# Optimization experiments

Measured on AMD Instinct MI355X. Metric: run time of the kernel, lower is better.

## Reference

```python
import jax, jax.numpy as jnp
import numpy as np

T, H, I, E, K = 1024, 1024, 512, 32, 4   # tokens, hidden, moe_inter, n_experts, top_k
G, TG, NS = 8, 4, 2                      # n_group, topk_group, n_shared_experts
C = 2 * T * K // E                       # expert capacity (no-drop headroom)
SCALE = 2.5                              # routed_scaling_factor


def setup_inputs() -> dict:
    key = jax.random.key(0)
    ks = jax.random.split(key, 7)
    s = 0.02
    return dict(
        hidden_states=jax.random.normal(ks[0], (T, H), jnp.float32),
        gate_w=jax.random.normal(ks[1], (E, H), jnp.float32) * s,
        e_bias=jax.random.normal(ks[2], (E,), jnp.float32) * 0.1,
        w_gate_up=jax.random.normal(ks[3], (E, 2 * I, H), jnp.float32) * s,
        w_down=jax.random.normal(ks[4], (E, H, I), jnp.float32) * s,
        w_gate_up_shared=jax.random.normal(ks[5], (2 * I * NS, H), jnp.float32) * s,
        w_down_shared=jax.random.normal(ks[6], (H, I * NS), jnp.float32) * s,
    )


def reference(hidden_states, gate_w, e_bias, w_gate_up, w_down, w_gate_up_shared, w_down_shared):
    x = hidden_states                                   # (T, H)
    # --- gate + sigmoid scoring (noaux_tc) ---
    logits = x @ gate_w.T                               # (T, E)
    scores = jax.nn.sigmoid(logits.astype(jnp.float32))
    sfc = scores + e_bias                               # scores_for_choice
    # --- group-limited top-k: top-2 sum per group, keep topk_group groups ---
    group_scores = jax.lax.top_k(sfc.reshape(T, G, E // G), 2)[0].sum(-1)  # (T, G)
    grp_idx = jax.lax.top_k(group_scores, TG)[1]        # (T, TG)
    gmask = jnp.zeros((T, G), jnp.float32).at[jnp.arange(T)[:, None], grp_idx].set(1.0)
    smask = jnp.repeat(gmask, E // G, axis=1)           # (T, E)
    sfc_m = jnp.where(smask > 0, sfc, 0.0)
    topk_idx = jax.lax.top_k(sfc_m, K)[1]               # (T, K)
    tw = jnp.take_along_axis(scores, topk_idx, axis=1)  # weights from raw scores
    tw = tw / (tw.sum(-1, keepdims=True) + 1e-20)       # norm_topk_prob
    tw = tw * SCALE
    # --- capacity-based dispatch (position within expert via cumsum of one-hot) ---
    e_flat = topk_idx.reshape(-1)                       # (T*K,)
    oh = jax.nn.one_hot(e_flat, E, dtype=jnp.float32)   # (T*K, E)
    pos = jnp.sum((jnp.cumsum(oh, axis=0) - 1.0) * oh, axis=-1).astype(jnp.int32)
    keep = (pos < C).astype(jnp.float32)                # capacity sized to never drop
    pos_c = jnp.clip(pos, 0, C - 1)
    t_flat = jnp.repeat(jnp.arange(T), K)
    combine = jnp.zeros((T, E, C), jnp.float32).at[t_flat, e_flat, pos_c].add(tw.reshape(-1) * keep)
    dispatch = jnp.zeros((T, E, C), jnp.float32).at[t_flat, e_flat, pos_c].add(keep)
    # --- grouped expert MLP (gate_up -> SiluAndMul -> down) ---
    xe = jnp.einsum('tec,th->ech', dispatch, x)         # (E, C, H)
    gu = jnp.einsum('ech,eoh->eco', xe, w_gate_up)      # (E, C, 2I)
    act = jax.nn.silu(gu[..., :I]) * gu[..., I:]
    ye = jnp.einsum('eci,ehi->ech', act, w_down)        # (E, C, H)
    routed = jnp.einsum('tec,ech->th', combine, ye)     # (T, H)
    # --- shared experts MLP on residual ---
    IS = I * NS
    gus = x @ w_gate_up_shared.T                        # (T, 2*IS)
    acts = jax.nn.silu(gus[:, :IS]) * gus[:, IS:]
    shared = acts @ w_down_shared.T                     # (T, H)
    return routed + shared
```

## Files before the change

### kernel.cpp

```cpp
#include <hip/hip_runtime.h>
#include <hip/hip_bf16.h>
#include <math.h>

#define T_TOK 1024
#define H_DIM 1024
#define I_DIM 512
#define E_NUM 32
#define K_TOP 4
#define G_NUM 8
#define TG_NUM 4
#define CAP 256
#define IS_DIM 1024
#define RSCALE 2.5f

#define MAXTILES 36

#define WS_CNT_OFF    0
#define WS_NT_OFF     128
#define WS_TILE_OFF   256
#define WS_EIDX_OFF   4096
#define WS_WN_OFF     20480
#define WS_STOK_OFF   36864
#define WS_SW_OFF     69632
#define WS_ACT_OFF    102400
#define WS_ACTS_OFF   (102400 + (size_t)E_NUM*CAP*I_DIM*2)
#define WS_XB_OFF     (WS_ACTS_OFF + (size_t)T_TOK*IS_DIM*2)
#define WS_T2S_OFF    (WS_XB_OFF + (size_t)T_TOK*H_DIM*2)
#define WS_YR_OFF     (WS_T2S_OFF + (size_t)T_TOK*K_TOP*4)

typedef __attribute__((ext_vector_type(8))) short short8v;
typedef __attribute__((ext_vector_type(4))) float f32x4;
typedef __attribute__((ext_vector_type(4))) unsigned uint4v;

__device__ __forceinline__ short f2bf(float f) {
    unsigned u = __float_as_uint(f);
    u += 0x7FFFu + ((u >> 16) & 1u);
    return (short)(u >> 16);
}
__device__ __forceinline__ unsigned pk2bf(float a, float b) {
    unsigned ua = __float_as_uint(a) + 0x8000u;
    unsigned ub = __float_as_uint(b) + 0x8000u;
    return __builtin_amdgcn_perm(ub, ua, 0x07060302);
}
__device__ __forceinline__ uint4v pk8bf(float4 lo, float4 hi) {
    uint4v r; r.x = pk2bf(lo.x, lo.y); r.y = pk2bf(lo.z, lo.w);
    r.z = pk2bf(hi.x, hi.y); r.w = pk2bf(hi.z, hi.w); return r;
}
__device__ __forceinline__ float silu_(float g) { return g / (1.f + expf(-g)); }

#define BAR_RELAXED() do { \
    asm volatile("s_waitcnt lgkmcnt(0)" ::: "memory"); \
    __builtin_amdgcn_s_barrier(); \
    asm volatile("" ::: "memory"); \
} while (0)

#define LDSTRIDE 40

__global__ __launch_bounds__(256) void gate_kernel(
    const float* __restrict__ x, const float* __restrict__ gate_w,
    const float* __restrict__ e_bias,
    int* __restrict__ eidx, float* __restrict__ wnorm, short* __restrict__ xb)
{
    __shared__ float xs[H_DIM];
    __shared__ float logits[E_NUM];
    const int t = blockIdx.x;
    const int tid = threadIdx.x;
    float4 v = ((const float4*)(x + (size_t)t * H_DIM))[tid];
    ((float4*)xs)[tid] = v;
    {
        unsigned* xd = (unsigned*)(xb + (size_t)t * H_DIM) + tid * 2;
        xd[0] = pk2bf(v.x, v.y); xd[1] = pk2bf(v.z, v.w);
    }
    __syncthreads();

    const int e = tid >> 3, sub = tid & 7;
    const float4* gw4 = (const float4*)(gate_w + (size_t)e * H_DIM + sub * 128);
    const float4* xr4 = (const float4*)(xs + sub * 128);
    float p = 0.f;
    #pragma unroll
    for (int h = 0; h < 32; ++h) {
        float4 a = xr4[h], b = gw4[h];
        p += a.x * b.x + a.y * b.y + a.z * b.z + a.w * b.w;
    }
    for (int off = 4; off; off >>= 1) p += __shfl_down(p, off, 8);
    if (sub == 0) logits[e] = p;
    __syncthreads();
    if (tid != 0) return;

    float sc[E_NUM], sfc[E_NUM];
    for (int i = 0; i < E_NUM; ++i) {
        sc[i] = 1.f / (1.f + expf(-logits[i]));
        sfc[i] = sc[i] + e_bias[i];
    }
    float gs[G_NUM];
    for (int g = 0; g < G_NUM; ++g) {
        float m1 = -1e30f, m2 = -1e30f;
        for (int j = 0; j < E_NUM / G_NUM; ++j) {
            float v2 = sfc[g * (E_NUM / G_NUM) + j];
            if (v2 > m1) { m2 = m1; m1 = v2; } else if (v2 > m2) m2 = v2;
        }
        gs[g] = m1 + m2;
    }
    bool gm[G_NUM];
    for (int g = 0; g < G_NUM; ++g) gm[g] = false;
    for (int it = 0; it < TG_NUM; ++it) {
        int best = -1; float bv = -1e30f;
        for (int g = 0; g < G_NUM; ++g) if (!gm[g] && gs[g] > bv) { bv = gs[g]; best = g; }
        gm[best] = true;
    }
    float sm[E_NUM];
    for (int i = 0; i < E_NUM; ++i) sm[i] = gm[i / (E_NUM / G_NUM)] ? sfc[i] : 0.0f;
    int idx[K_TOP]; float w[K_TOP]; float tsum = 0.f;
    for (int it = 0; it < K_TOP; ++it) {
        int best = 0; float bv = -1e30f;
        for (int i = 0; i < E_NUM; ++i) if (sm[i] > bv) { bv = sm[i]; best = i; }
        sm[best] = -1e30f;
        idx[it] = best; w[it] = sc[best]; tsum += w[it];
    }
    float inv = RSCALE / (tsum + 1e-20f);
    const int base = t * K_TOP;
    for (int it = 0; it < K_TOP; ++it) {
        eidx[base + it] = idx[it];
        wnorm[base + it] = w[it] * inv;
    }
}

__global__ __launch_bounds__(256) void assign_kernel(
    const int* __restrict__ eidx, const float* __restrict__ wnorm,
    int* __restrict__ cnt, int* __restrict__ slot_token, float* __restrict__ slot_w,
    int* __restrict__ ntiles, int* __restrict__ tiles, int* __restrict__ tok2slot)
{
    __shared__ int   se[T_TOK * K_TOP];
    __shared__ float swt[T_TOK * K_TOP];
    __shared__ int   scnt[E_NUM];
    const int tid = threadIdx.x;
    for (int i = tid; i < T_TOK * K_TOP; i += 256) { se[i] = eidx[i]; swt[i] = wnorm[i]; }
    __syncthreads();

    const int e = tid >> 3;
    const int seg = tid & 7;
    const int base = seg * 512;
    int c = 0;
    for (int i = 0; i < 512; ++i) c += (se[base + i] == e);
    int excl = 0, total = 0;
    for (int s = 0; s < 8; ++s) {
        int cs = __shfl(c, s, 8);
        total += cs;
        if (s < seg) excl += cs;
    }
    if (seg == 0) { cnt[e] = total; scnt[e] = total; }
    __syncthreads();
    int boff = 0;
    for (int ee = 0; ee < e; ++ee) boff += min(scnt[ee], CAP);

    int pos = excl;
    for (int i = 0; i < 512; ++i) {
        if (se[base + i] == e) {
            const int g = base + i;
            if (pos < CAP) {
                slot_token[e * CAP + pos] = g >> 2;
                slot_w[e * CAP + pos] = swt[g];
                tok2slot[g] = boff + pos;
            } else {
                tok2slot[g] = -1;
            }
            ++pos;
        }
    }
    __syncthreads();
    if (tid == 0) {
        int nt = 0;
        for (int t0 = 0; t0 < T_TOK; t0 += 256) {
            tiles[nt * 4] = -1; tiles[nt * 4 + 1] = t0; tiles[nt * 4 + 2] = 256;
            tiles[nt * 4 + 3] = 0; ++nt;
        }
        int off = 0;
        for (int ee = 0; ee < E_NUM; ++ee) {
            int n = min(scnt[ee], CAP);
            if (n > 0) {
                tiles[nt * 4] = ee; tiles[nt * 4 + 1] = 0; tiles[nt * 4 + 2] = n;
                tiles[nt * 4 + 3] = off; ++nt;
            }
            off += n;
        }
        *ntiles = nt;
    }
}


__global__ __launch_bounds__(512, 2) void gu_all_kernel(
    const short* __restrict__ xb, const float* __restrict__ w_gate_up,
    const float* __restrict__ w_gus,
    const int* __restrict__ ntiles, const int* __restrict__ tiles,
    const int* __restrict__ slot_token, const float* __restrict__ slot_w,
    short* __restrict__ act, short* __restrict__ acts)
{
    if ((int)blockIdx.y >= *ntiles) return;
    const int e  = tiles[blockIdx.y * 4];
    const int r0 = tiles[blockIdx.y * 4 + 1];
    const int ne = tiles[blockIdx.y * 4 + 2];
    const bool sh = (e < 0);
    if (!sh && blockIdx.x >= I_DIM / 64) return;
    const int col0 = blockIdx.x * 64;
    const int mchunks = (ne + 63) >> 6;
    const int rows = mchunks << 6;

    __shared__ __align__(16) short As[2][256 * LDSTRIDE];
    __shared__ __align__(16) short Bs[2][128 * LDSTRIDE];
    __shared__ int   toks[256];
    __shared__ float sws[256];

    const int tid = threadIdx.x;
    const int lane = tid & 63, wid = tid >> 6;
    const int wm = wid & 3, wn = wid >> 2;
    const int lr16 = lane & 15, kc = lane >> 4;
    const int sc_ = tid & 3, srow = tid >> 2;

    if (tid < 256) {
        if (sh) { toks[tid] = r0 + tid; sws[tid] = 1.f; }
        else {
            bool v = tid < ne;
            toks[tid] = v ? slot_token[e * CAP + tid] : 0;
            sws[tid]  = v ? slot_w[e * CAP + tid] : 0.f;
        }
    }
    __syncthreads();

    const int IDim = sh ? IS_DIM : I_DIM;
    const float* wbase = sh ? w_gus : (w_gate_up + (size_t)e * (2 * I_DIM) * H_DIM);
    const int wr = ((srow >> 4) & 1) * IDim + col0 + ((srow >> 5) << 4) + (srow & 15);
    const float* bptr = wbase + (size_t)wr * H_DIM + sc_ * 8;
    const bool a0v = srow < rows;
    const bool a1v = (srow + 128) < rows;
    const short* aptr0 = xb + (size_t)toks[srow] * H_DIM + sc_ * 8;
    const short* aptr1 = xb + (size_t)toks[srow + 128] * H_DIM + sc_ * 8;
    const int aoff0 = srow * LDSTRIDE + sc_ * 8;
    const int aoff1 = (srow + 128) * LDSTRIDE + sc_ * 8;
    const int boff  = srow * LDSTRIDE + sc_ * 8;

    f32x4 acc[4][4];
    #pragma unroll
    for (int i = 0; i < 4; ++i)
        #pragma unroll
        for (int j = 0; j < 4; ++j) acc[i][j] = 0.f;

    short8v cA0{}, cA1{};
    if (a0v) cA0 = *(const short8v*)(aptr0);
    if (a1v) cA1 = *(const short8v*)(aptr1);
    float4 cB0 = *(const float4*)(bptr), cB1 = *(const float4*)(bptr + 4);

    int buf = 0;
    for (int k0 = 0; k0 < H_DIM; k0 += 32) {
        short8v nA0{}, nA1{};
        float4 nB0{}, nB1{};
        const int k1 = k0 + 32;
        if (k1 < H_DIM) {
            if (a0v) nA0 = *(const short8v*)(aptr0 + k1);
            if (a1v) nA1 = *(const short8v*)(aptr1 + k1);
            nB0 = *(const float4*)(bptr + k1); nB1 = *(const float4*)(bptr + k1 + 4);
        }
        if (a0v) *(short8v*)&As[buf][aoff0] = cA0;
        if (a1v) *(short8v*)&As[buf][aoff1] = cA1;
        *(uint4v*)&Bs[buf][boff] = pk8bf(cB0, cB1);
        BAR_RELAXED();
        if (wm < mchunks) {
            short8v a_[4], b_[4];
            #pragma unroll
            for (int mt = 0; mt < 4; ++mt)
                a_[mt] = *(const short8v*)&As[buf][(wm * 64 + mt * 16 + lr16) * LDSTRIDE + kc * 8];
            #pragma unroll
            for (int nt = 0; nt < 4; ++nt)
                b_[nt] = *(const short8v*)&Bs[buf][(wn * 64 + nt * 16 + lr16) * LDSTRIDE + kc * 8];
            #pragma unroll
            for (int mt = 0; mt < 4; ++mt)
                #pragma unroll
                for (int nt = 0; nt < 4; ++nt)
                    acc[mt][nt] = __builtin_amdgcn_mfma_f32_16x16x32_bf16(a_[mt], b_[nt], acc[mt][nt], 0, 0, 0);
        }
        buf ^= 1;
        cA0 = nA0; cA1 = nA1; cB0 = nB0; cB1 = nB1;
    }

    if (wm >= mchunks) return;
    #pragma unroll
    for (int mt = 0; mt < 4; ++mt) {
        #pragma unroll
        for (int q = 0; q < 2; ++q) {
            f32x4 g = acc[mt][2 * q], u = acc[mt][2 * q + 1];
            const int colI = col0 + wn * 32 + q * 16 + lr16;
            #pragma unroll
            for (int i = 0; i < 4; ++i) {
                int r = wm * 64 + mt * 16 + kc * 4 + i;
                if (r < ne) {
                    float s = sws[r];
                    short* dst = sh ? (acts + (size_t)(r0 + r) * IS_DIM + colI)
                                    : (act + ((size_t)e * CAP + r) * I_DIM + colI);
                    *dst = f2bf(s * silu_(g[i]) * u[i]);
                }
            }
        }
    }
}

__global__ __launch_bounds__(512, 2) void down_all_kernel(
    const short* __restrict__ act, const short* __restrict__ acts,
    const float* __restrict__ w_down, const float* __restrict__ w_ds,
    const int* __restrict__ ntiles, const int* __restrict__ tiles,
    float* __restrict__ yr, float* __restrict__ out)
{
    if ((int)blockIdx.y >= *ntiles) return;
    const int e  = tiles[blockIdx.y * 4];
    const int r0 = tiles[blockIdx.y * 4 + 1];
    const int ne = tiles[blockIdx.y * 4 + 2];
    const int bo = tiles[blockIdx.y * 4 + 3];
    const bool sh = (e < 0);
    const int h0 = blockIdx.x * 128;
    const int mchunks = (ne + 63) >> 6;
    const int rows = mchunks << 6;

    __shared__ __align__(16) short As[2][256 * LDSTRIDE];
    __shared__ __align__(16) short Bs[2][128 * LDSTRIDE];

    const int tid = threadIdx.x;
    const int lane = tid & 63, wid = tid >> 6;
    const int wm = wid & 3, wn = wid >> 2;
    const int lr16 = lane & 15, kc = lane >> 4;
    const int sc_ = tid & 3, srow = tid >> 2;

    const int Kdim = sh ? IS_DIM : I_DIM;
    const short* abase = sh ? (acts + (size_t)r0 * IS_DIM) : (act + (size_t)e * CAP * I_DIM);
    const float* wbase = sh ? w_ds : (w_down + (size_t)e * H_DIM * I_DIM);
    const float* bptr  = wbase + (size_t)(h0 + srow) * Kdim + sc_ * 8;
    const bool a0v = srow < rows;
    const bool a1v = (srow + 128) < rows;
    const short* aptr0 = abase + (size_t)srow * Kdim + sc_ * 8;
    const short* aptr1 = abase + (size_t)(srow + 128) * Kdim + sc_ * 8;
    const int aoff0 = srow * LDSTRIDE + sc_ * 8;
    const int aoff1 = (srow + 128) * LDSTRIDE + sc_ * 8;
    const int boff  = srow * LDSTRIDE + sc_ * 8;

    f32x4 acc[4][4];
    #pragma unroll
    for (int i = 0; i < 4; ++i)
        #pragma unroll
        for (int j = 0; j < 4; ++j) acc[i][j] = 0.f;

    short8v cA0{}, cA1{};
    if (a0v) cA0 = *(const short8v*)(aptr0);
    if (a1v) cA1 = *(const short8v*)(aptr1);
    float4 cB0 = *(const float4*)(bptr), cB1 = *(const float4*)(bptr + 4);

    int buf = 0;
    for (int k0 = 0; k0 < Kdim; k0 += 32) {
        short8v nA0{}, nA1{};
        float4 nB0{}, nB1{};
        const int k1 = k0 + 32;
        if (k1 < Kdim) {
            if (a0v) nA0 = *(const short8v*)(aptr0 + k1);
            if (a1v) nA1 = *(const short8v*)(aptr1 + k1);
            nB0 = *(const float4*)(bptr + k1); nB1 = *(const float4*)(bptr + k1 + 4);
        }
        if (a0v) *(short8v*)&As[buf][aoff0] = cA0;
        if (a1v) *(short8v*)&As[buf][aoff1] = cA1;
        *(uint4v*)&Bs[buf][boff] = pk8bf(cB0, cB1);
        BAR_RELAXED();
        if (wm < mchunks) {
            short8v a_[4], b_[4];
            #pragma unroll
            for (int mt = 0; mt < 4; ++mt)
                a_[mt] = *(const short8v*)&As[buf][(wm * 64 + mt * 16 + lr16) * LDSTRIDE + kc * 8];
            #pragma unroll
            for (int nt = 0; nt < 4; ++nt)
                b_[nt] = *(const short8v*)&Bs[buf][(wn * 64 + nt * 16 + lr16) * LDSTRIDE + kc * 8];
            #pragma unroll
            for (int mt = 0; mt < 4; ++mt)
                #pragma unroll
                for (int nt = 0; nt < 4; ++nt)
                    acc[mt][nt] = __builtin_amdgcn_mfma_f32_16x16x32_bf16(a_[mt], b_[nt], acc[mt][nt], 0, 0, 0);
        }
        buf ^= 1;
        cA0 = nA0; cA1 = nA1; cB0 = nB0; cB1 = nB1;
    }

    if (wm >= mchunks) return;
    #pragma unroll
    for (int mt = 0; mt < 4; ++mt) {
        #pragma unroll
        for (int i = 0; i < 4; ++i) {
            int r = wm * 64 + mt * 16 + kc * 4 + i;
            if (r < ne) {
                float* orow = sh ? (out + (size_t)(r0 + r) * H_DIM + h0 + wn * 64)
                                 : (yr + (size_t)(bo + r) * H_DIM + h0 + wn * 64);
                #pragma unroll
                for (int nt = 0; nt < 4; ++nt)
                    orow[nt * 16 + lr16] = acc[mt][nt][i];
            }
        }
    }
}

__global__ __launch_bounds__(256) void combine_kernel(
    const float* __restrict__ yr, const int* __restrict__ tok2slot,
    float* __restrict__ out)
{
    const int t = blockIdx.x, tid = threadIdx.x;
    float4 a = ((const float4*)(out + (size_t)t * H_DIM))[tid];
    #pragma unroll
    for (int k = 0; k < K_TOP; ++k) {
        int s = tok2slot[t * K_TOP + k];
        if (s >= 0) {
            float4 b = ((const float4*)(yr + (size_t)s * H_DIM))[tid];
            a.x += b.x; a.y += b.y; a.z += b.z; a.w += b.w;
        }
    }
    ((float4*)(out + (size_t)t * H_DIM))[tid] = a;
}

extern "C" void kernel_launch(void* const* d_in, const int* in_sizes, int n_in,
                              void* d_out, int out_size, void* d_ws, size_t ws_size,
                              hipStream_t stream) {
    const float* x   = (const float*)d_in[0];
    const float* gw  = (const float*)d_in[1];
    const float* eb  = (const float*)d_in[2];
    const float* wgu = (const float*)d_in[3];
    const float* wd  = (const float*)d_in[4];
    const float* wgs = (const float*)d_in[5];
    const float* wds = (const float*)d_in[6];
    float* out = (float*)d_out;
    char* ws = (char*)d_ws;

    int*   cnt    = (int*)(ws + WS_CNT_OFF);
    int*   ntiles = (int*)(ws + WS_NT_OFF);
    int*   tiles  = (int*)(ws + WS_TILE_OFF);
    int*   eidx   = (int*)(ws + WS_EIDX_OFF);
    float* wnorm  = (float*)(ws + WS_WN_OFF);
    int*   stok   = (int*)(ws + WS_STOK_OFF);
    float* sw     = (float*)(ws + WS_SW_OFF);
    short* act    = (short*)(ws + WS_ACT_OFF);
    short* acts   = (short*)(ws + WS_ACTS_OFF);
    short* xb     = (short*)(ws + WS_XB_OFF);
    int*   t2s    = (int*)(ws + WS_T2S_OFF);
    float* yr     = (float*)(ws + WS_YR_OFF);

    gate_kernel<<<T_TOK, 256, 0, stream>>>(x, gw, eb, eidx, wnorm, xb);
    assign_kernel<<<1, 256, 0, stream>>>(eidx, wnorm, cnt, stok, sw, ntiles, tiles, t2s);
    gu_all_kernel<<<dim3(IS_DIM / 64, MAXTILES), 512, 0, stream>>>(
        xb, wgu, wgs, ntiles, tiles, stok, sw, act, acts);
    down_all_kernel<<<dim3(H_DIM / 128, MAXTILES), 512, 0, stream>>>(
        act, acts, wd, wds, ntiles, tiles, yr, out);
    combine_kernel<<<T_TOK, 256, 0, stream>>>(yr, t2s, out);
}
```

Before: 440.7 us.

## Split expert tiles into 128-row chunks with BK=64 and higher occupancy

Changes the tile scheduler to emit 128-row tiles for both shared and routed experts, so an expert with more than 128 slots becomes several tiles and more blocks run. Both GEMM kernels move from a 256x128 block tile to 128x128 with a 2x4 warp layout, a K-step of 64 and LDS stride 72, and launch bounds allow 4 blocks per CU. Rows are no longer masked per 64-row chunk: loads always run, which depends on padding rows in the token and activation buffers being safe to read. The aim is better load balance and occupancy, at the cost of more redundant weight reads across row tiles.

```diff
diff --git a/kernel.cpp b/kernel.cpp
--- a/kernel.cpp
+++ b/kernel.cpp
@@ -13,7 +13,7 @@
 #define IS_DIM 1024
 #define RSCALE 2.5f
 
-#define MAXTILES 36
+#define MAXTILES 72
 
 #define WS_CNT_OFF    0
 #define WS_NT_OFF     128
@@ -54,7 +54,7 @@
     asm volatile("" ::: "memory"); \
 } while (0)
 
-#define LDSTRIDE 40
+#define LDSTRIDE 72
 
 __global__ __launch_bounds__(256) void gate_kernel(
     const float* __restrict__ x, const float* __restrict__ gate_w,
@@ -170,16 +170,17 @@
     __syncthreads();
     if (tid == 0) {
         int nt = 0;
-        for (int t0 = 0; t0 < T_TOK; t0 += 256) {
-            tiles[nt * 4] = -1; tiles[nt * 4 + 1] = t0; tiles[nt * 4 + 2] = 256;
+        for (int t0 = 0; t0 < T_TOK; t0 += 128) {
+            tiles[nt * 4] = -1; tiles[nt * 4 + 1] = t0; tiles[nt * 4 + 2] = 128;
             tiles[nt * 4 + 3] = 0; ++nt;
         }
         int off = 0;
         for (int ee = 0; ee < E_NUM; ++ee) {
             int n = min(scnt[ee], CAP);
-            if (n > 0) {
-                tiles[nt * 4] = ee; tiles[nt * 4 + 1] = 0; tiles[nt * 4 + 2] = n;
-                tiles[nt * 4 + 3] = off; ++nt;
+            for (int r = 0; r < n; r += 128) {
+                tiles[nt * 4] = ee; tiles[nt * 4 + 1] = r;
+                tiles[nt * 4 + 2] = min(128, n - r);
+                tiles[nt * 4 + 3] = off + r; ++nt;
             }
             off += n;
         }
@@ -188,7 +189,33 @@
 }
 
 
-__global__ __launch_bounds__(512, 2) void gu_all_kernel(
+#define GEMM_SETUP() \
+    const int tid = threadIdx.x; \
+    const int lane = tid & 63, wid = tid >> 6; \
+    const int wm = wid & 1, wn = wid >> 1; \
+    const int lr16 = lane & 15, kc = lane >> 4; \
+    const int sc_ = tid & 7, srow = tid >> 3; \
+    const int aoff0 = srow * LDSTRIDE + sc_ * 8; \
+    const int aoff1 = (srow + 64) * LDSTRIDE + sc_ * 8;
+
+#define DECL_ACC42() f32x4 acc[4][2]; \
+    _Pragma("unroll") for (int i_ = 0; i_ < 4; ++i_) \
+    _Pragma("unroll") for (int j_ = 0; j_ < 2; ++j_) acc[i_][j_] = 0.f;
+
+#define COMPUTE_BK64(Asb, Bsb) do { \
+    _Pragma("unroll") for (int ks = 0; ks < 2; ++ks) { \
+        short8v a_[4], b_[2]; \
+        _Pragma("unroll") for (int mt = 0; mt < 4; ++mt) \
+            a_[mt] = *(const short8v*)&(Asb)[(wm*64 + mt*16 + lr16)*LDSTRIDE + ks*32 + kc*8]; \
+        _Pragma("unroll") for (int nt = 0; nt < 2; ++nt) \
+            b_[nt] = *(const short8v*)&(Bsb)[(wn*32 + nt*16 + lr16)*LDSTRIDE + ks*32 + kc*8]; \
+        _Pragma("unroll") for (int mt = 0; mt < 4; ++mt) \
+        _Pragma("unroll") for (int nt = 0; nt < 2; ++nt) \
+            acc[mt][nt] = __builtin_amdgcn_mfma_f32_16x16x32_bf16(a_[mt], b_[nt], acc[mt][nt], 0, 0, 0); \
+    } \
+} while (0)
+
+__global__ __launch_bounds__(512, 4) void gu_all_kernel(
     const short* __restrict__ xb, const float* __restrict__ w_gate_up,
     const float* __restrict__ w_gus,
     const int* __restrict__ ntiles, const int* __restrict__ tiles,
@@ -202,107 +229,77 @@
     const bool sh = (e < 0);
     if (!sh && blockIdx.x >= I_DIM / 64) return;
     const int col0 = blockIdx.x * 64;
-    const int mchunks = (ne + 63) >> 6;
-    const int rows = mchunks << 6;
-
-    __shared__ __align__(16) short As[2][256 * LDSTRIDE];
+
+    __shared__ __align__(16) short As[2][128 * LDSTRIDE];
     __shared__ __align__(16) short Bs[2][128 * LDSTRIDE];
-    __shared__ int   toks[256];
-    __shared__ float sws[256];
-
-    const int tid = threadIdx.x;
-    const int lane = tid & 63, wid = tid >> 6;
-    const int wm = wid & 3, wn = wid >> 2;
-    const int lr16 = lane & 15, kc = lane >> 4;
-    const int sc_ = tid & 3, srow = tid >> 2;
-
-    if (tid < 256) {
+    __shared__ int   toks[128];
+    __shared__ float sws[128];
+
+    GEMM_SETUP();
+    if (tid < 128) {
         if (sh) { toks[tid] = r0 + tid; sws[tid] = 1.f; }
         else {
             bool v = tid < ne;
-            toks[tid] = v ? slot_token[e * CAP + tid] : 0;
-            sws[tid]  = v ? slot_w[e * CAP + tid] : 0.f;
+            toks[tid] = v ? slot_token[e * CAP + r0 + tid] : 0;
+            sws[tid]  = v ? slot_w[e * CAP + r0 + tid] : 0.f;
         }
     }
     __syncthreads();
 
     const int IDim = sh ? IS_DIM : I_DIM;
     const float* wbase = sh ? w_gus : (w_gate_up + (size_t)e * (2 * I_DIM) * H_DIM);
-    const int wr = ((srow >> 4) & 1) * IDim + col0 + ((srow >> 5) << 4) + (srow & 15);
-    const float* bptr = wbase + (size_t)wr * H_DIM + sc_ * 8;
-    const bool a0v = srow < rows;
-    const bool a1v = (srow + 128) < rows;
-    const short* aptr0 = xb + (size_t)toks[srow] * H_DIM + sc_ * 8;
-    const short* aptr1 = xb + (size_t)toks[srow + 128] * H_DIM + sc_ * 8;
-    const int aoff0 = srow * LDSTRIDE + sc_ * 8;
-    const int aoff1 = (srow + 128) * LDSTRIDE + sc_ * 8;
-    const int boff  = srow * LDSTRIDE + sc_ * 8;
-
-    f32x4 acc[4][4];
-    #pragma unroll
-    for (int i = 0; i < 4; ++i)
-        #pragma unroll
-        for (int j = 0; j < 4; ++j) acc[i][j] = 0.f;
-
-    short8v cA0{}, cA1{};
-    if (a0v) cA0 = *(const short8v*)(aptr0);
-    if (a1v) cA1 = *(const short8v*)(aptr1);
-    float4 cB0 = *(const float4*)(bptr), cB1 = *(const float4*)(bptr + 4);
+    const int r_0 = srow, r_1 = srow + 64;
+    const int wr0 = ((r_0 >> 4) & 1) * IDim + col0 + ((r_0 >> 5) << 4) + (r_0 & 15);
+    const int wr1 = ((r_1 >> 4) & 1) * IDim + col0 + ((r_1 >> 5) << 4) + (r_1 & 15);
+    const float* bptr0 = wbase + (size_t)wr0 * H_DIM + sc_ * 8;
+    const float* bptr1 = wbase + (size_t)wr1 * H_DIM + sc_ * 8;
+    const short* aptr0 = xb + (size_t)toks[r_0] * H_DIM + sc_ * 8;
+    const short* aptr1 = xb + (size_t)toks[r_1] * H_DIM + sc_ * 8;
+
+    DECL_ACC42();
+    short8v cA0 = *(const short8v*)(aptr0), cA1 = *(const short8v*)(aptr1);
+    float4 cB0a = *(const float4*)(bptr0), cB0b = *(const float4*)(bptr0 + 4);
+    float4 cB1a = *(const float4*)(bptr1), cB1b = *(const float4*)(bptr1 + 4);
 
     int buf = 0;
-    for (int k0 = 0; k0 < H_DIM; k0 += 32) {
+    for (int k0 = 0; k0 < H_DIM; k0 += 64) {
         short8v nA0{}, nA1{};
-        float4 nB0{}, nB1{};
-        const int k1 = k0 + 32;
+        float4 nB0a{}, nB0b{}, nB1a{}, nB1b{};
+        const int k1 = k0 + 64;
         if (k1 < H_DIM) {
-            if (a0v) nA0 = *(const short8v*)(aptr0 + k1);
-            if (a1v) nA1 = *(const short8v*)(aptr1 + k1);
-            nB0 = *(const float4*)(bptr + k1); nB1 = *(const float4*)(bptr + k1 + 4);
-        }
-        if (a0v) *(short8v*)&As[buf][aoff0] = cA0;
-        if (a1v) *(short8v*)&As[buf][aoff1] = cA1;
-        *(uint4v*)&Bs[buf][boff] = pk8bf(cB0, cB1);
+            nA0 = *(const short8v*)(aptr0 + k1);  nA1 = *(const short8v*)(aptr1 + k1);
+            nB0a = *(const float4*)(bptr0 + k1);  nB0b = *(const float4*)(bptr0 + k1 + 4);
+            nB1a = *(const float4*)(bptr1 + k1);  nB1b = *(const float4*)(bptr1 + k1 + 4);
+        }
+        *(short8v*)&As[buf][aoff0] = cA0;
+        *(short8v*)&As[buf][aoff1] = cA1;
+        *(uint4v*)&Bs[buf][aoff0]  = pk8bf(cB0a, cB0b);
+        *(uint4v*)&Bs[buf][aoff1]  = pk8bf(cB1a, cB1b);
         BAR_RELAXED();
-        if (wm < mchunks) {
-            short8v a_[4], b_[4];
-            #pragma unroll
-            for (int mt = 0; mt < 4; ++mt)
-                a_[mt] = *(const short8v*)&As[buf][(wm * 64 + mt * 16 + lr16) * LDSTRIDE + kc * 8];
-            #pragma unroll
-            for (int nt = 0; nt < 4; ++nt)
-                b_[nt] = *(const short8v*)&Bs[buf][(wn * 64 + nt * 16 + lr16) * LDSTRIDE + kc * 8];
-            #pragma unroll
-            for (int mt = 0; mt < 4; ++mt)
-                #pragma unroll
-                for (int nt = 0; nt < 4; ++nt)
-                    acc[mt][nt] = __builtin_amdgcn_mfma_f32_16x16x32_bf16(a_[mt], b_[nt], acc[mt][nt], 0, 0, 0);
-        }
+        COMPUTE_BK64(As[buf], Bs[buf]);
         buf ^= 1;
-        cA0 = nA0; cA1 = nA1; cB0 = nB0; cB1 = nB1;
-    }
-
-    if (wm >= mchunks) return;
+        cA0 = nA0; cA1 = nA1;
+        cB0a = nB0a; cB0b = nB0b; cB1a = nB1a; cB1b = nB1b;
+    }
+
     #pragma unroll
     for (int mt = 0; mt < 4; ++mt) {
+        f32x4 g = acc[mt][0], u = acc[mt][1];
+        const int colI = col0 + wn * 16 + lr16;
         #pragma unroll
-        for (int q = 0; q < 2; ++q) {
-            f32x4 g = acc[mt][2 * q], u = acc[mt][2 * q + 1];
-            const int colI = col0 + wn * 32 + q * 16 + lr16;
-            #pragma unroll
-            for (int i = 0; i < 4; ++i) {
-                int r = wm * 64 + mt * 16 + kc * 4 + i;
-                if (r < ne) {
-                    float s = sws[r];
-                    short* dst = sh ? (acts + (size_t)(r0 + r) * IS_DIM + colI)
-                                    : (act + ((size_t)e * CAP + r) * I_DIM + colI);
-                    *dst = f2bf(s * silu_(g[i]) * u[i]);
-                }
+        for (int i = 0; i < 4; ++i) {
+            int r = wm * 64 + mt * 16 + kc * 4 + i;
+            if (r < ne) {
+                float s = sws[r];
+                short* dst = sh ? (acts + (size_t)(r0 + r) * IS_DIM + colI)
+                                : (act + ((size_t)e * CAP + r0 + r) * I_DIM + colI);
+                *dst = f2bf(s * silu_(g[i]) * u[i]);
             }
         }
     }
 }
 
-__global__ __launch_bounds__(512, 2) void down_all_kernel(
+__global__ __launch_bounds__(512, 4) void down_all_kernel(
     const short* __restrict__ act, const short* __restrict__ acts,
     const float* __restrict__ w_down, const float* __restrict__ w_ds,
     const int* __restrict__ ntiles, const int* __restrict__ tiles,
@@ -315,84 +312,57 @@
     const int bo = tiles[blockIdx.y * 4 + 3];
     const bool sh = (e < 0);
     const int h0 = blockIdx.x * 128;
-    const int mchunks = (ne + 63) >> 6;
-    const int rows = mchunks << 6;
-
-    __shared__ __align__(16) short As[2][256 * LDSTRIDE];
+
+    __shared__ __align__(16) short As[2][128 * LDSTRIDE];
     __shared__ __align__(16) short Bs[2][128 * LDSTRIDE];
 
-    const int tid = threadIdx.x;
-    const int lane = tid & 63, wid = tid >> 6;
-    const int wm = wid & 3, wn = wid >> 2;
-    const int lr16 = lane & 15, kc = lane >> 4;
-    const int sc_ = tid & 3, srow = tid >> 2;
+    GEMM_SETUP();
 
     const int Kdim = sh ? IS_DIM : I_DIM;
-    const short* abase = sh ? (acts + (size_t)r0 * IS_DIM) : (act + (size_t)e * CAP * I_DIM);
+    const short* abase = sh ? (acts + (size_t)r0 * IS_DIM)
+                            : (act + ((size_t)e * CAP + r0) * I_DIM);
     const float* wbase = sh ? w_ds : (w_down + (size_t)e * H_DIM * I_DIM);
-    const float* bptr  = wbase + (size_t)(h0 + srow) * Kdim + sc_ * 8;
-    const bool a0v = srow < rows;
-    const bool a1v = (srow + 128) < rows;
+    const float* bptr0 = wbase + (size_t)(h0 + srow) * Kdim + sc_ * 8;
+    const float* bptr1 = wbase + (size_t)(h0 + srow + 64) * Kdim + sc_ * 8;
     const short* aptr0 = abase + (size_t)srow * Kdim + sc_ * 8;
-    const short* aptr1 = abase + (size_t)(srow + 128) * Kdim + sc_ * 8;
-    const int aoff0 = srow * LDSTRIDE + sc_ * 8;
-    const int aoff1 = (srow + 128) * LDSTRIDE + sc_ * 8;
-    const int boff  = srow * LDSTRIDE + sc_ * 8;
-
-    f32x4 acc[4][4];
-    #pragma unroll
-    for (int i = 0; i < 4; ++i)
-        #pragma unroll
-        for (int j = 0; j < 4; ++j) acc[i][j] = 0.f;
-
-    short8v cA0{}, cA1{};
-    if (a0v) cA0 = *(const short8v*)(aptr0);
-    if (a1v) cA1 = *(const short8v*)(aptr1);
-    float4 cB0 = *(const float4*)(bptr), cB1 = *(const float4*)(bptr + 4);
+    const short* aptr1 = abase + (size_t)(srow + 64) * Kdim + sc_ * 8;
+
+    DECL_ACC42();
+    short8v cA0 = *(const short8v*)(aptr0), cA1 = *(const short8v*)(aptr1);
+    float4 cB0a = *(const float4*)(bptr0), cB0b = *(const float4*)(bptr0 + 4);
+    float4 cB1a = *(const float4*)(bptr1), cB1b = *(const float4*)(bptr1 + 4);
 
     int buf = 0;
-    for (int k0 = 0; k0 < Kdim; k0 += 32) {
+    for (int k0 = 0; k0 < Kdim; k0 += 64) {
         short8v nA0{}, nA1{};
-        float4 nB0{}, nB1{};
-        const int k1 = k0 + 32;
+        float4 nB0a{}, nB0b{}, nB1a{}, nB1b{};
+        const int k1 = k0 + 64;
         if (k1 < Kdim) {
-            if (a0v) nA0 = *(const short8v*)(aptr0 + k1);
-            if (a1v) nA1 = *(const short8v*)(aptr1 + k1);
-            nB0 = *(const float4*)(bptr + k1); nB1 = *(const float4*)(bptr + k1 + 4);
-        }
-        if (a0v) *(short8v*)&As[buf][aoff0] = cA0;
-        if (a1v) *(short8v*)&As[buf][aoff1] = cA1;
-        *(uint4v*)&Bs[buf][boff] = pk8bf(cB0, cB1);
+            nA0 = *(const short8v*)(aptr0 + k1);  nA1 = *(const short8v*)(aptr1 + k1);
+            nB0a = *(const float4*)(bptr0 + k1);  nB0b = *(const float4*)(bptr0 + k1 + 4);
+            nB1a = *(const float4*)(bptr1 + k1);  nB1b = *(const float4*)(bptr1 + k1 + 4);
+        }
+        *(short8v*)&As[buf][aoff0] = cA0;
+        *(short8v*)&As[buf][aoff1] = cA1;
+        *(uint4v*)&Bs[buf][aoff0]  = pk8bf(cB0a, cB0b);
+        *(uint4v*)&Bs[buf][aoff1]  = pk8bf(cB1a, cB1b);
         BAR_RELAXED();
-        if (wm < mchunks) {
-            short8v a_[4], b_[4];
-            #pragma unroll
-            for (int mt = 0; mt < 4; ++mt)
-                a_[mt] = *(const short8v*)&As[buf][(wm * 64 + mt * 16 + lr16) * LDSTRIDE + kc * 8];
-            #pragma unroll
-            for (int nt = 0; nt < 4; ++nt)
-                b_[nt] = *(const short8v*)&Bs[buf][(wn * 64 + nt * 16 + lr16) * LDSTRIDE + kc * 8];
-            #pragma unroll
-            for (int mt = 0; mt < 4; ++mt)
-                #pragma unroll
-                for (int nt = 0; nt < 4; ++nt)
-                    acc[mt][nt] = __builtin_amdgcn_mfma_f32_16x16x32_bf16(a_[mt], b_[nt], acc[mt][nt], 0, 0, 0);
-        }
+        COMPUTE_BK64(As[buf], Bs[buf]);
         buf ^= 1;
-        cA0 = nA0; cA1 = nA1; cB0 = nB0; cB1 = nB1;
-    }
-
-    if (wm >= mchunks) return;
+        cA0 = nA0; cA1 = nA1;
+        cB0a = nB0a; cB0b = nB0b; cB1a = nB1a; cB1b = nB1b;
+    }
+
     #pragma unroll
     for (int mt = 0; mt < 4; ++mt) {
         #pragma unroll
         for (int i = 0; i < 4; ++i) {
             int r = wm * 64 + mt * 16 + kc * 4 + i;
             if (r < ne) {
-                float* orow = sh ? (out + (size_t)(r0 + r) * H_DIM + h0 + wn * 64)
-                                 : (yr + (size_t)(bo + r) * H_DIM + h0 + wn * 64);
+                float* orow = sh ? (out + (size_t)(r0 + r) * H_DIM + h0 + wn * 32)
+                                 : (yr + (size_t)(bo + r) * H_DIM + h0 + wn * 32);
                 #pragma unroll
-                for (int nt = 0; nt < 4; ++nt)
+                for (int nt = 0; nt < 2; ++nt)
                     orow[nt * 16 + lr16] = acc[mt][nt][i];
             }
         }
```

Measured after the change: 400.5 us. 9.1% less time.
